# Kernel tuning notes

Hardware: AMD Instinct MI355X
Metric: run time of the kernel (lower is better)

The kernel has to match this reference:

```python
import jax, jax.numpy as jnp
import numpy as np

B, C, H, W = 8, 256, 64, 64
OUT, K = 256, 3
OG = 1
STRIDE, PAD, DIL = 1, 1, 1
K2 = K * K


def setup_inputs() -> dict:
    key = jax.random.key(0)
    ks = jax.random.split(key, 5)
    x = jax.random.normal(ks[0], (B, C, H, W), jnp.float32)
    # main deform-conv weight [out, in//groups, k, k]
    weight = jax.random.normal(ks[1], (OUT, C, K, K), jnp.float32) * (1.0 / np.sqrt(C * K2))
    bias = jax.random.normal(ks[2], (OUT,), jnp.float32) * 0.01
    # param_generator: 3x3 conv -> 3*OG*K*K channels (oh, ow, mask)
    pg_w = jax.random.normal(ks[3], (3 * OG * K2, C, 3, 3), jnp.float32) * 0.01
    pg_b = jax.random.normal(ks[4], (3 * OG * K2,), jnp.float32) * 0.01
    return {"x": x, "weight": weight, "bias": bias, "pg_w": pg_w, "pg_b": pg_b}


def _conv3x3(x, w, b):
    y = jax.lax.conv_general_dilated(
        x, w, (1, 1), [(1, 1), (1, 1)],
        dimension_numbers=("NCHW", "OIHW", "NCHW"))
    return y + b[None, :, None, None]


def _bilinear_gather(img, py, px):
    # img [B,C,H,W]; py,px [B,K2,Ho,Wo] -> [B,C,K2,Ho,Wo]
    # Zero padding outside the image (torchvision deform_conv2d semantics).
    Hh, Ww = img.shape[2], img.shape[3]
    y0 = jnp.floor(py)
    x0 = jnp.floor(px)
    dy = py - y0
    dx = px - x0
    imgf = img.reshape(img.shape[0], img.shape[1], Hh * Ww)
    out = jnp.zeros((img.shape[0], img.shape[1]) + py.shape[1:], img.dtype)
    corners = (
        (0, 0, (1 - dy) * (1 - dx)),
        (0, 1, (1 - dy) * dx),
        (1, 0, dy * (1 - dx)),
        (1, 1, dy * dx),
    )
    for oy, ox, wgt in corners:
        yy = y0 + oy
        xx = x0 + ox
        valid = (yy >= 0) & (yy < Hh) & (xx >= 0) & (xx < Ww)
        yi = jnp.clip(yy, 0, Hh - 1).astype(jnp.int32)
        xi = jnp.clip(xx, 0, Ww - 1).astype(jnp.int32)
        idx = yi * Ww + xi  # [B,K2,Ho,Wo]
        g = jax.vmap(lambda im, ix: jnp.take(im, ix.reshape(-1), axis=1))(imgf, idx)
        g = g.reshape(img.shape[0], img.shape[1], *idx.shape[1:])
        out = out + g * (wgt * valid)[:, None]
    return out


def _deform_conv2d(x, weight, bias, pg_w, pg_b):
    Bn = x.shape[0]
    Hi, Wi = x.shape[2], x.shape[3]
    Ho = (Hi + 2 * PAD - DIL * (K - 1) - 1) // STRIDE + 1
    Wo = (Wi + 2 * PAD - DIL * (K - 1) - 1) // STRIDE + 1
    params = _conv3x3(x, pg_w, pg_b)  # [B, 3*OG*K2, H, W]
    oh, ow, mask = jnp.split(params, 3, axis=1)
    offset = jnp.concatenate([oh, ow], axis=1)  # [B, 2*OG*K2, Ho, Wo]
    mask = jax.nn.sigmoid(mask)                  # [B, OG*K2, Ho, Wo]
    # torchvision layout: channel = ((og*K2 + k)*2 + {y,x})
    off = offset.reshape(Bn, OG, K2, 2, Ho, Wo)
    dy = off[:, :, :, 0].reshape(Bn, K2, Ho, Wo)  # OG == 1
    dx = off[:, :, :, 1].reshape(Bn, K2, Ho, Wo)
    hy = jnp.arange(Ho, dtype=x.dtype) * STRIDE - PAD
    wx = jnp.arange(Wo, dtype=x.dtype) * STRIDE - PAD
    ky, kx = jnp.meshgrid(jnp.arange(K), jnp.arange(K), indexing="ij")
    base_y = hy[None, :, None] + (ky.reshape(-1) * DIL).astype(x.dtype)[:, None, None]  # [K2,Ho,1]
    base_x = wx[None, None, :] + (kx.reshape(-1) * DIL).astype(x.dtype)[:, None, None]  # [K2,1,Wo]
    py = dy + base_y[None]  # [B,K2,Ho,Wo]
    px = dx + base_x[None]
    sampled = _bilinear_gather(x, py, px)          # [B,C,K2,Ho,Wo]
    sampled = sampled * mask[:, None]              # modulation (OG=1)
    out = jnp.einsum("bckhw,ock->bohw", sampled, weight.reshape(OUT, C, K2))
    return out + bias[None, :, None, None]


def reference(x, weight, bias, pg_w, pg_b):
    return _deform_conv2d(x, weight, bias, pg_w, pg_b)
```

## Files before the change

kernel.cpp:

```cpp
#include <hip/hip_runtime.h>
#include <math.h>

#define BQ   8
#define CIN  256
#define HH   64
#define WW   64
#define COUT 256
#define K2   9
#define PCH  27

#define PT     64
#define CCH    32
#define NCHUNK (CIN / CCH)
#define NSTEP  72
#define NSUB   24
#define SUBROW 104
#define PLANE  (HH * WW)

typedef __attribute__((ext_vector_type(8))) short short8;
typedef __attribute__((ext_vector_type(4))) float f32x4;
typedef __attribute__((ext_vector_type(2))) float f32x2;

#define PIPE_BARRIER() do {                                   \
    asm volatile("s_waitcnt lgkmcnt(0)" ::: "memory");        \
    __builtin_amdgcn_s_barrier();                             \
    asm volatile("" ::: "memory");                            \
} while (0)

static __device__ __forceinline__ unsigned short f2bf(float f) {
    unsigned u = __builtin_bit_cast(unsigned, f);
    u += 0x7fff + ((u >> 16) & 1);
    return (unsigned short)(u >> 16);
}
static __device__ __forceinline__ f32x2 up2(unsigned u) {
    f32x2 r;
    r[0] = __builtin_bit_cast(float, u << 16);
    r[1] = __builtin_bit_cast(float, u & 0xffff0000u);
    return r;
}
static __device__ __forceinline__ unsigned cvtpk(float lo, float hi) {
    unsigned r;
    asm("v_cvt_pk_bf16_f32 %0, %1, %2" : "=v"(r) : "v"(lo), "v"(hi));
    return r;
}

__global__ __launch_bounds__(256) void k_packw(const float* __restrict__ w,
                                               unsigned short* __restrict__ wp) {
    int t = blockIdx.x * 256 + threadIdx.x;
    if (t >= NSTEP * COUT * 4) return;
    int q = t & 3;
    int o = (t >> 2) & 255;
    int s = t >> 10;
    short8 sv;
#pragma unroll
    for (int j = 0; j < 8; ++j) {
        int pos   = s * 32 + q * 8 + j;
        int chunk = pos / (CCH * K2);
        int pl    = pos % (CCH * K2);
        int ktap  = pl >> 5;
        int c     = chunk * CCH + (pl & 31);
        sv[j] = (short)f2bf(w[(o * CIN + c) * K2 + ktap]);
    }
    *(short8*)(wp + (size_t)t * 8) = sv;
}

__global__ __launch_bounds__(256) void k_packpg(const float* __restrict__ pgw,
                                                unsigned short* __restrict__ wpg) {
    int t = blockIdx.x * 256 + threadIdx.x;
    if (t >= NSTEP * 32 * 4) return;
    int q = t & 3;
    int o = (t >> 2) & 31;
    int s = t >> 7;
    short8 sv;
#pragma unroll
    for (int j = 0; j < 8; ++j) {
        int pos   = s * 32 + q * 8 + j;
        int chunk = pos / (CCH * K2);
        int pl    = pos % (CCH * K2);
        int ktap  = pl >> 5;
        int c     = chunk * CCH + (pl & 31);
        sv[j] = (o < PCH) ? (short)f2bf(pgw[(size_t)(o * CIN + c) * K2 + ktap]) : (short)0;
    }
    *(short8*)(wpg + (size_t)t * 8) = sv;
}

__global__ __launch_bounds__(256) void k_xt(const float* __restrict__ x,
                                            unsigned short* __restrict__ xT) {
    __shared__ float tile[64][65];
    int blk = blockIdx.x;
    int cc  = blk & 3;
    int y   = (blk >> 2) & 63;
    int b   = blk >> 8;
    int t   = threadIdx.x;
    int c0  = cc * 64;

    const float* xp = x + ((size_t)(b * CIN + c0) * HH + y) * WW;
#pragma unroll
    for (int r = 0; r < 16; ++r) {
        int cl = r * 4 + (t >> 6);
        int xx = t & 63;
        tile[cl][xx] = xp[(size_t)cl * PLANE + xx];
    }
    __syncthreads();
    unsigned short* op = xT + ((size_t)b * PLANE + (size_t)y * WW) * CIN + c0;
#pragma unroll
    for (int r = 0; r < 16; ++r) {
        int xx = r * 4 + (t >> 6);
        int cl = t & 63;
        op[(size_t)xx * CIN + cl] = f2bf(tile[cl][xx]);
    }
}

__global__ __launch_bounds__(512, 4) void k_fused(const unsigned short* __restrict__ xT,
                                                  const unsigned short* __restrict__ wp,
                                                  const unsigned short* __restrict__ wpg,
                                                  const float* __restrict__ bias,
                                                  const float* __restrict__ pgb,
                                                  float* __restrict__ out) {
    __shared__ alignas(16) unsigned short s_samp[2][PT][SUBROW];
    __shared__ float4 s_wgt4[K2][PT];
    __shared__ int4   s_off4[K2][PT];
    __shared__ float  s_params[32][65];

    int blk = blockIdx.x;
    int swz = (blk & 7) * 64 + (blk >> 3);
    int b   = swz >> 6;
    int h   = swz & 63;
    int t   = threadIdx.x;

    int gp = t >> 3;
    int cg = t & 7;
    int wv = t >> 6;
    int lm = t & 15;
    int lq = (t >> 4) & 3;

    const char* xTb = (const char*)xT + (size_t)b * PLANE * CIN * 2;

    {
        int ipg = wv >> 2;
        int rpg = wv & 3;
        f32x4 accA = (f32x4){0.f, 0.f, 0.f, 0.f};
        f32x4 accB = (f32x4){0.f, 0.f, 0.f, 0.f};

        int  pixo[K2];
        bool okk[K2];
#pragma unroll
        for (int k = 0; k < K2; ++k) {
            int row = h + (k / 3) - 1;
            int col = gp + (k % 3) - 1;
            okk[k]  = ((unsigned)row < (unsigned)HH) & ((unsigned)col < (unsigned)WW);
            int pix = min(max(row, 0), HH - 1) * WW + min(max(col, 0), WW - 1);
            pixo[k] = pix * (CIN * 2) + cg * 8;
        }

        uint2 Ga[3];
#pragma unroll
        for (int j = 0; j < 3; ++j)
            Ga[j] = *(const uint2*)(xTb + pixo[j]);
#pragma unroll
        for (int j = 0; j < 3; ++j) {
            uint2 d = Ga[j];
            if (!okk[j]) { d.x = 0; d.y = 0; }
            *(uint2*)&s_samp[0][gp][j * 32 + cg * 4] = d;
        }
#pragma unroll
        for (int j = 0; j < 3; ++j)
            Ga[j] = *(const uint2*)(xTb + pixo[3 + j]);
        PIPE_BARRIER();

        short8 ac = *(const short8*)(wpg + (ipg * 16 + lm) * 32 + lq * 8);
        for (int sc = 0; sc < NSUB; ++sc) {
            bool doC = (sc + 1 < NSUB);
            bool doL = (sc + 2 < NSUB);
            int t1 = ((sc + 1) % 3) * 3;
            int t2 = ((sc + 2) % 3) * 3;
            int c2 = ((sc + 2) / 3) * (CCH * 2);
            unsigned short (*__restrict__ bc)[SUBROW] = s_samp[sc & 1];
            unsigned short (*__restrict__ bn)[SUBROW] = s_samp[(sc + 1) & 1];
#pragma unroll
            for (int sl = 0; sl < 3; ++sl) {
                short8 bf = *(const short8*)&bc[rpg * 16 + lm][sl * 32 + lq * 8];
                int r = sc * 3 + sl + 1;
                short8 an = ac;
                if (r < NSTEP)
                    an = *(const short8*)(wpg + (size_t)r * 32 * 32
                                          + (ipg * 16 + lm) * 32 + lq * 8);
                if (doC) {
                    uint2 d = Ga[sl];
                    if (!okk[t1 + sl]) { d.x = 0; d.y = 0; }
                    *(uint2*)&bn[gp][sl * 32 + cg * 4] = d;
                }
                if (doL)
                    Ga[sl] = *(const uint2*)(xTb + pixo[t2 + sl] + c2);
                if (sl & 1)
                    accB = __builtin_amdgcn_mfma_f32_16x16x32_bf16(ac, bf, accB, 0, 0, 0);
                else
                    accA = __builtin_amdgcn_mfma_f32_16x16x32_bf16(ac, bf, accA, 0, 0, 0);
                ac = an;
            }
            PIPE_BARRIER();
        }
        f32x4 accpg = accA + accB;
#pragma unroll
        for (int rg = 0; rg < 4; ++rg) {
            int oc = ipg * 16 + lq * 4 + rg;
            float bb = (oc < PCH) ? pgb[oc] : 0.f;
            s_params[oc][rpg * 16 + lm] = accpg[rg] + bb;
        }
    }
    __syncthreads();

    for (int e = t; e < K2 * PT; e += 512) {
        int k = e >> 6;
        int p = e & 63;
        float dy = s_params[2 * k][p];
        float dx = s_params[2 * k + 1][p];
        float mz = s_params[18 + k][p];
        float m  = 1.f / (1.f + expf(-mz));

        float py = dy + (float)(h - 1 + k / 3);
        float px = dx + (float)(p - 1 + k % 3);
        float y0f = floorf(py), x0f = floorf(px);
        float fy = py - y0f,    fx = px - x0f;
        int iy0 = (int)y0f, ix0 = (int)x0f;
        int iy1 = iy0 + 1,  ix1 = ix0 + 1;
        bool vy0 = (unsigned)iy0 < (unsigned)HH;
        bool vy1 = (unsigned)iy1 < (unsigned)HH;
        bool vx0 = (unsigned)ix0 < (unsigned)WW;
        bool vx1 = (unsigned)ix1 < (unsigned)WW;

        float w00 = (1.f - fy) * (1.f - fx) * m; if (!(vy0 && vx0)) w00 = 0.f;
        float w01 = (1.f - fy) * fx         * m; if (!(vy0 && vx1)) w01 = 0.f;
        float w10 = fy         * (1.f - fx) * m; if (!(vy1 && vx0)) w10 = 0.f;
        float w11 = fy         * fx         * m; if (!(vy1 && vx1)) w11 = 0.f;

        int cy0 = min(max(iy0, 0), HH - 1), cy1 = min(max(iy1, 0), HH - 1);
        int cx0 = min(max(ix0, 0), WW - 1), cx1 = min(max(ix1, 0), WW - 1);

        s_wgt4[k][p] = make_float4(w00, w01, w10, w11);
        s_off4[k][p] = make_int4((cy0 * WW + cx0) * 512, (cy0 * WW + cx1) * 512,
                                 (cy1 * WW + cx0) * 512, (cy1 * WW + cx1) * 512);
    }
    __syncthreads();

    int ow = wv * 32;
    f32x4 acc[2][4];
#pragma unroll
    for (int i = 0; i < 2; ++i)
#pragma unroll
        for (int j = 0; j < 4; ++j) acc[i][j] = (f32x4){0.f, 0.f, 0.f, 0.f};

    uint2 G[3][4];
    {
#pragma unroll
        for (int j = 0; j < 3; ++j) {
            int4 ob = s_off4[j][gp];
            G[j][0] = *(const uint2*)(xTb + ob.x + cg * 8);
            G[j][1] = *(const uint2*)(xTb + ob.y + cg * 8);
            G[j][2] = *(const uint2*)(xTb + ob.z + cg * 8);
            G[j][3] = *(const uint2*)(xTb + ob.w + cg * 8);
        }
#pragma unroll
        for (int j = 0; j < 3; ++j) {
            float4 gw = s_wgt4[j][gp];
            f32x2 v01 = gw.x * up2(G[j][0].x) + gw.y * up2(G[j][1].x)
                      + gw.z * up2(G[j][2].x) + gw.w * up2(G[j][3].x);
            f32x2 v23 = gw.x * up2(G[j][0].y) + gw.y * up2(G[j][1].y)
                      + gw.z * up2(G[j][2].y) + gw.w * up2(G[j][3].y);
            uint2 pk;
            pk.x = cvtpk(v01[0], v01[1]);
            pk.y = cvtpk(v23[0], v23[1]);
            *(uint2*)&s_samp[0][gp][j * 32 + cg * 4] = pk;
        }
#pragma unroll
        for (int j = 0; j < 3; ++j) {
            int4 ob = s_off4[3 + j][gp];
            G[j][0] = *(const uint2*)(xTb + ob.x + cg * 8);
            G[j][1] = *(const uint2*)(xTb + ob.y + cg * 8);
            G[j][2] = *(const uint2*)(xTb + ob.z + cg * 8);
            G[j][3] = *(const uint2*)(xTb + ob.w + cg * 8);
        }
        PIPE_BARRIER();
    }

    short8 a0c = *(const short8*)(wp + (ow +  0 + lm) * 32 + lq * 8);
    short8 a1c = *(const short8*)(wp + (ow + 16 + lm) * 32 + lq * 8);
    for (int sc = 0; sc < NSUB; ++sc) {
        bool doC = (sc + 1 < NSUB);
        bool doL = (sc + 2 < NSUB);
        int t1 = ((sc + 1) % 3) * 3;
        int t2 = ((sc + 2) % 3) * 3;
        int c2 = ((sc + 2) / 3) * (CCH * 2) + cg * 8;
        unsigned short (*__restrict__ bc)[SUBROW] = s_samp[sc & 1];
        unsigned short (*__restrict__ bn)[SUBROW] = s_samp[(sc + 1) & 1];
#pragma unroll
        for (int sl = 0; sl < 3; ++sl) {
            short8 b0 = *(const short8*)&bc[ 0 + lm][sl * 32 + lq * 8];
            short8 b1 = *(const short8*)&bc[16 + lm][sl * 32 + lq * 8];
            short8 b2 = *(const short8*)&bc[32 + lm][sl * 32 + lq * 8];
            short8 b3 = *(const short8*)&bc[48 + lm][sl * 32 + lq * 8];
            int r = sc * 3 + sl + 1;
            short8 a0n = a0c, a1n = a1c;
            if (r < NSTEP) {
                const unsigned short* wrn = wp + (size_t)r * COUT * 32;
                a0n = *(const short8*)(wrn + (ow +  0 + lm) * 32 + lq * 8);
                a1n = *(const short8*)(wrn + (ow + 16 + lm) * 32 + lq * 8);
            }
            if (doC) {
                float4 gw = s_wgt4[t1 + sl][gp];
                f32x2 v01 = gw.x * up2(G[sl][0].x) + gw.y * up2(G[sl][1].x)
                          + gw.z * up2(G[sl][2].x) + gw.w * up2(G[sl][3].x);
                f32x2 v23 = gw.x * up2(G[sl][0].y) + gw.y * up2(G[sl][1].y)
                          + gw.z * up2(G[sl][2].y) + gw.w * up2(G[sl][3].y);
                uint2 pk;
                pk.x = cvtpk(v01[0], v01[1]);
                pk.y = cvtpk(v23[0], v23[1]);
                *(uint2*)&bn[gp][sl * 32 + cg * 4] = pk;
            }
            if (doL) {
                int4 ob = s_off4[t2 + sl][gp];
                G[sl][0] = *(const uint2*)(xTb + ob.x + c2);
                G[sl][1] = *(const uint2*)(xTb + ob.y + c2);
                G[sl][2] = *(const uint2*)(xTb + ob.z + c2);
                G[sl][3] = *(const uint2*)(xTb + ob.w + c2);
            }
            __builtin_amdgcn_s_setprio(1);
            acc[0][0] = __builtin_amdgcn_mfma_f32_16x16x32_bf16(a0c, b0, acc[0][0], 0, 0, 0);
            acc[0][1] = __builtin_amdgcn_mfma_f32_16x16x32_bf16(a0c, b1, acc[0][1], 0, 0, 0);
            acc[0][2] = __builtin_amdgcn_mfma_f32_16x16x32_bf16(a0c, b2, acc[0][2], 0, 0, 0);
            acc[0][3] = __builtin_amdgcn_mfma_f32_16x16x32_bf16(a0c, b3, acc[0][3], 0, 0, 0);
            acc[1][0] = __builtin_amdgcn_mfma_f32_16x16x32_bf16(a1c, b0, acc[1][0], 0, 0, 0);
            acc[1][1] = __builtin_amdgcn_mfma_f32_16x16x32_bf16(a1c, b1, acc[1][1], 0, 0, 0);
            acc[1][2] = __builtin_amdgcn_mfma_f32_16x16x32_bf16(a1c, b2, acc[1][2], 0, 0, 0);
            acc[1][3] = __builtin_amdgcn_mfma_f32_16x16x32_bf16(a1c, b3, acc[1][3], 0, 0, 0);
            __builtin_amdgcn_s_setprio(0);
            a0c = a0n; a1c = a1n;
        }
        PIPE_BARRIER();
    }

    float* op = out + ((size_t)b * COUT) * PLANE + h * WW;
#pragma unroll
    for (int i = 0; i < 2; ++i) {
        int o0 = ow + i * 16 + lq * 4;
        f32x4 bv = *(const f32x4*)(bias + o0);
#pragma unroll
        for (int rg = 0; rg < 4; ++rg) {
#pragma unroll
            for (int j = 0; j < 4; ++j)
                op[(size_t)(o0 + rg) * PLANE + j * 16 + lm] = acc[i][j][rg] + bv[rg];
        }
    }
}

extern "C" void kernel_launch(void* const* d_in, const int* in_sizes, int n_in,
                              void* d_out, int out_size, void* d_ws, size_t ws_size,
                              hipStream_t stream) {
    const float* x    = (const float*)d_in[0];
    const float* wgt  = (const float*)d_in[1];
    const float* bias = (const float*)d_in[2];
    const float* pgw  = (const float*)d_in[3];
    const float* pgb  = (const float*)d_in[4];
    float* out = (float*)d_out;

    const size_t WPK_B = (size_t)NSTEP * COUT * 32 * 2;
    const size_t WPG_B = (size_t)NSTEP * 32 * 32 * 2;
    unsigned short* wpk = (unsigned short*)d_ws;
    unsigned short* wpg = (unsigned short*)((char*)d_ws + WPK_B);
    unsigned short* xT  = (unsigned short*)((char*)d_ws + WPK_B + WPG_B);

    k_packw <<<(NSTEP * COUT * 4 + 255) / 256, 256, 0, stream>>>(wgt, wpk);
    k_packpg<<<(NSTEP * 32 * 4 + 255) / 256,   256, 0, stream>>>(pgw, wpg);
    k_xt    <<<BQ * HH * 4, 256, 0, stream>>>(x, xT);
    k_fused <<<BQ * HH, 512, 0, stream>>>(xT, wpk, wpg, bias, pgb, out);
}
```

Before: 120.2 us.

## Retile MFMA warp tiles to 64 outputs x 32 pixels and shrink gather registers

Each wave now covers 64 output channels by 32 pixels instead of 32 by 64. That cuts LDS B-fragment reads per step but doubles the weight A-fragment global loads, which are no longer prefetched one step ahead. The bilinear weights are hoisted into registers, and the gather buffer is cut from three sets of corner loads to one, with a reordered loop. The aim is lower register pressure and LDS traffic. The cost is gather and weight-load latency that is less hidden behind the MFMAs.

```diff
diff --git a/kernel.cpp b/kernel.cpp
--- a/kernel.cpp
+++ b/kernel.cpp
@@ -243,111 +243,125 @@
     }
     __syncthreads();
 
-    int ow = wv * 32;
-    f32x4 acc[2][4];
-#pragma unroll
-    for (int i = 0; i < 2; ++i)
-#pragma unroll
-        for (int j = 0; j < 4; ++j) acc[i][j] = (f32x4){0.f, 0.f, 0.f, 0.f};
-
-    uint2 G[3][4];
+    int ow  = (wv >> 1) * 64;
+    int pxt = (wv & 1) * 32;
+    f32x4 acc[4][2];
+#pragma unroll
+    for (int i = 0; i < 4; ++i)
+#pragma unroll
+        for (int j = 0; j < 2; ++j) acc[i][j] = (f32x4){0.f, 0.f, 0.f, 0.f};
+
+    f32x4 wreg[K2];
+#pragma unroll
+    for (int k = 0; k < K2; ++k)
+        wreg[k] = *(const f32x4*)&s_wgt4[k][gp];
+
+    uint2 G[4];
     {
+        uint2 Gp[3][4];
 #pragma unroll
         for (int j = 0; j < 3; ++j) {
             int4 ob = s_off4[j][gp];
-            G[j][0] = *(const uint2*)(xTb + ob.x + cg * 8);
-            G[j][1] = *(const uint2*)(xTb + ob.y + cg * 8);
-            G[j][2] = *(const uint2*)(xTb + ob.z + cg * 8);
-            G[j][3] = *(const uint2*)(xTb + ob.w + cg * 8);
+            Gp[j][0] = *(const uint2*)(xTb + ob.x + cg * 8);
+            Gp[j][1] = *(const uint2*)(xTb + ob.y + cg * 8);
+            Gp[j][2] = *(const uint2*)(xTb + ob.z + cg * 8);
+            Gp[j][3] = *(const uint2*)(xTb + ob.w + cg * 8);
         }
 #pragma unroll
         for (int j = 0; j < 3; ++j) {
-            float4 gw = s_wgt4[j][gp];
-            f32x2 v01 = gw.x * up2(G[j][0].x) + gw.y * up2(G[j][1].x)
-                      + gw.z * up2(G[j][2].x) + gw.w * up2(G[j][3].x);
-            f32x2 v23 = gw.x * up2(G[j][0].y) + gw.y * up2(G[j][1].y)
-                      + gw.z * up2(G[j][2].y) + gw.w * up2(G[j][3].y);
+            f32x4 gw = wreg[j];
+            f32x2 v01 = gw[0] * up2(Gp[j][0].x) + gw[1] * up2(Gp[j][1].x)
+                      + gw[2] * up2(Gp[j][2].x) + gw[3] * up2(Gp[j][3].x);
+            f32x2 v23 = gw[0] * up2(Gp[j][0].y) + gw[1] * up2(Gp[j][1].y)
+                      + gw[2] * up2(Gp[j][2].y) + gw[3] * up2(Gp[j][3].y);
             uint2 pk;
             pk.x = cvtpk(v01[0], v01[1]);
             pk.y = cvtpk(v23[0], v23[1]);
             *(uint2*)&s_samp[0][gp][j * 32 + cg * 4] = pk;
         }
-#pragma unroll
-        for (int j = 0; j < 3; ++j) {
-            int4 ob = s_off4[3 + j][gp];
-            G[j][0] = *(const uint2*)(xTb + ob.x + cg * 8);
-            G[j][1] = *(const uint2*)(xTb + ob.y + cg * 8);
-            G[j][2] = *(const uint2*)(xTb + ob.z + cg * 8);
-            G[j][3] = *(const uint2*)(xTb + ob.w + cg * 8);
+        {
+            int4 ob = s_off4[3][gp];
+            G[0] = *(const uint2*)(xTb + ob.x + cg * 8);
+            G[1] = *(const uint2*)(xTb + ob.y + cg * 8);
+            G[2] = *(const uint2*)(xTb + ob.z + cg * 8);
+            G[3] = *(const uint2*)(xTb + ob.w + cg * 8);
         }
         PIPE_BARRIER();
     }
 
-    short8 a0c = *(const short8*)(wp + (ow +  0 + lm) * 32 + lq * 8);
-    short8 a1c = *(const short8*)(wp + (ow + 16 + lm) * 32 + lq * 8);
-    for (int sc = 0; sc < NSUB; ++sc) {
-        bool doC = (sc + 1 < NSUB);
-        bool doL = (sc + 2 < NSUB);
-        int t1 = ((sc + 1) % 3) * 3;
-        int t2 = ((sc + 2) % 3) * 3;
-        int c2 = ((sc + 2) / 3) * (CCH * 2) + cg * 8;
-        unsigned short (*__restrict__ bc)[SUBROW] = s_samp[sc & 1];
-        unsigned short (*__restrict__ bn)[SUBROW] = s_samp[(sc + 1) & 1];
-#pragma unroll
-        for (int sl = 0; sl < 3; ++sl) {
-            short8 b0 = *(const short8*)&bc[ 0 + lm][sl * 32 + lq * 8];
-            short8 b1 = *(const short8*)&bc[16 + lm][sl * 32 + lq * 8];
-            short8 b2 = *(const short8*)&bc[32 + lm][sl * 32 + lq * 8];
-            short8 b3 = *(const short8*)&bc[48 + lm][sl * 32 + lq * 8];
-            int r = sc * 3 + sl + 1;
-            short8 a0n = a0c, a1n = a1c;
-            if (r < NSTEP) {
-                const unsigned short* wrn = wp + (size_t)r * COUT * 32;
-                a0n = *(const short8*)(wrn + (ow +  0 + lm) * 32 + lq * 8);
-                a1n = *(const short8*)(wrn + (ow + 16 + lm) * 32 + lq * 8);
+    for (int ch = 0; ch < NCHUNK; ++ch) {
+        const int chb = ch * (CCH * 2);
+#pragma unroll
+        for (int q = 0; q < 3; ++q) {
+            unsigned short (*__restrict__ bc)[SUBROW] = s_samp[(ch + q) & 1];
+            unsigned short (*__restrict__ bn)[SUBROW] = s_samp[(ch + q + 1) & 1];
+            const int T1 = ((q + 1) % 3) * 3;
+            const int cC = chb + ((q + 1) / 3) * (CCH * 2);
+            const int T2 = ((q + 2) % 3) * 3;
+            const int cL = chb + ((q + 2) / 3) * (CCH * 2);
+            const bool doC = (q < 2) || (ch < NCHUNK - 1);
+            const bool doL2 = (ch * 3 + q + 2) < NSUB;
+#pragma unroll
+            for (int sl = 0; sl < 3; ++sl) {
+                short8 b0 = *(const short8*)&bc[pxt +  0 + lm][sl * 32 + lq * 8];
+                short8 b1 = *(const short8*)&bc[pxt + 16 + lm][sl * 32 + lq * 8];
+                const unsigned short* wr = wp + (size_t)(ch * 9 + q * 3 + sl) * COUT * 32;
+                short8 a0 = *(const short8*)(wr + (ow +  0 + lm) * 32 + lq * 8);
+                short8 a1 = *(const short8*)(wr + (ow + 16 + lm) * 32 + lq * 8);
+                short8 a2 = *(const short8*)(wr + (ow + 32 + lm) * 32 + lq * 8);
+                short8 a3 = *(const short8*)(wr + (ow + 48 + lm) * 32 + lq * 8);
+                if (doC) {
+                    f32x4 gw = wreg[T1 + sl];
+                    f32x2 v01 = gw[0] * up2(G[0].x) + gw[1] * up2(G[1].x)
+                              + gw[2] * up2(G[2].x) + gw[3] * up2(G[3].x);
+                    f32x2 v23 = gw[0] * up2(G[0].y) + gw[1] * up2(G[1].y)
+                              + gw[2] * up2(G[2].y) + gw[3] * up2(G[3].y);
+                    uint2 pk;
+                    pk.x = cvtpk(v01[0], v01[1]);
+                    pk.y = cvtpk(v23[0], v23[1]);
+                    *(uint2*)&bn[gp][sl * 32 + cg * 4] = pk;
+                }
+                if (sl < 2) {
+                    if (doC) {
+                        int4 ob = s_off4[T1 + sl + 1][gp];
+                        G[0] = *(const uint2*)(xTb + ob.x + cC + cg * 8);
+                        G[1] = *(const uint2*)(xTb + ob.y + cC + cg * 8);
+                        G[2] = *(const uint2*)(xTb + ob.z + cC + cg * 8);
+                        G[3] = *(const uint2*)(xTb + ob.w + cC + cg * 8);
+                    }
+                } else {
+                    if (doL2) {
+                        int4 ob = s_off4[T2][gp];
+                        G[0] = *(const uint2*)(xTb + ob.x + cL + cg * 8);
+                        G[1] = *(const uint2*)(xTb + ob.y + cL + cg * 8);
+                        G[2] = *(const uint2*)(xTb + ob.z + cL + cg * 8);
+                        G[3] = *(const uint2*)(xTb + ob.w + cL + cg * 8);
+                    }
+                }
+                __builtin_amdgcn_s_setprio(1);
+                acc[0][0] = __builtin_amdgcn_mfma_f32_16x16x32_bf16(a0, b0, acc[0][0], 0, 0, 0);
+                acc[0][1] = __builtin_amdgcn_mfma_f32_16x16x32_bf16(a0, b1, acc[0][1], 0, 0, 0);
+                acc[1][0] = __builtin_amdgcn_mfma_f32_16x16x32_bf16(a1, b0, acc[1][0], 0, 0, 0);
+                acc[1][1] = __builtin_amdgcn_mfma_f32_16x16x32_bf16(a1, b1, acc[1][1], 0, 0, 0);
+                acc[2][0] = __builtin_amdgcn_mfma_f32_16x16x32_bf16(a2, b0, acc[2][0], 0, 0, 0);
+                acc[2][1] = __builtin_amdgcn_mfma_f32_16x16x32_bf16(a2, b1, acc[2][1], 0, 0, 0);
+                acc[3][0] = __builtin_amdgcn_mfma_f32_16x16x32_bf16(a3, b0, acc[3][0], 0, 0, 0);
+                acc[3][1] = __builtin_amdgcn_mfma_f32_16x16x32_bf16(a3, b1, acc[3][1], 0, 0, 0);
+                __builtin_amdgcn_s_setprio(0);
             }
-            if (doC) {
-                float4 gw = s_wgt4[t1 + sl][gp];
-                f32x2 v01 = gw.x * up2(G[sl][0].x) + gw.y * up2(G[sl][1].x)
-                          + gw.z * up2(G[sl][2].x) + gw.w * up2(G[sl][3].x);
-                f32x2 v23 = gw.x * up2(G[sl][0].y) + gw.y * up2(G[sl][1].y)
-                          + gw.z * up2(G[sl][2].y) + gw.w * up2(G[sl][3].y);
-                uint2 pk;
-                pk.x = cvtpk(v01[0], v01[1]);
-                pk.y = cvtpk(v23[0], v23[1]);
-                *(uint2*)&bn[gp][sl * 32 + cg * 4] = pk;
-            }
-            if (doL) {
-                int4 ob = s_off4[t2 + sl][gp];
-                G[sl][0] = *(const uint2*)(xTb + ob.x + c2);
-                G[sl][1] = *(const uint2*)(xTb + ob.y + c2);
-                G[sl][2] = *(const uint2*)(xTb + ob.z + c2);
-                G[sl][3] = *(const uint2*)(xTb + ob.w + c2);
-            }
-            __builtin_amdgcn_s_setprio(1);
-            acc[0][0] = __builtin_amdgcn_mfma_f32_16x16x32_bf16(a0c, b0, acc[0][0], 0, 0, 0);
-            acc[0][1] = __builtin_amdgcn_mfma_f32_16x16x32_bf16(a0c, b1, acc[0][1], 0, 0, 0);
-            acc[0][2] = __builtin_amdgcn_mfma_f32_16x16x32_bf16(a0c, b2, acc[0][2], 0, 0, 0);
-            acc[0][3] = __builtin_amdgcn_mfma_f32_16x16x32_bf16(a0c, b3, acc[0][3], 0, 0, 0);
-            acc[1][0] = __builtin_amdgcn_mfma_f32_16x16x32_bf16(a1c, b0, acc[1][0], 0, 0, 0);
-            acc[1][1] = __builtin_amdgcn_mfma_f32_16x16x32_bf16(a1c, b1, acc[1][1], 0, 0, 0);
-            acc[1][2] = __builtin_amdgcn_mfma_f32_16x16x32_bf16(a1c, b2, acc[1][2], 0, 0, 0);
-            acc[1][3] = __builtin_amdgcn_mfma_f32_16x16x32_bf16(a1c, b3, acc[1][3], 0, 0, 0);
-            __builtin_amdgcn_s_setprio(0);
-            a0c = a0n; a1c = a1n;
-        }
-        PIPE_BARRIER();
-    }
-
-    float* op = out + ((size_t)b * COUT) * PLANE + h * WW;
-#pragma unroll
-    for (int i = 0; i < 2; ++i) {
+            PIPE_BARRIER();
+        }
+    }
+
+    float* op = out + ((size_t)b * COUT) * PLANE + h * WW + pxt;
+#pragma unroll
+    for (int i = 0; i < 4; ++i) {
         int o0 = ow + i * 16 + lq * 4;
         f32x4 bv = *(const f32x4*)(bias + o0);
 #pragma unroll
         for (int rg = 0; rg < 4; ++rg) {
 #pragma unroll
-            for (int j = 0; j < 4; ++j)
+            for (int j = 0; j < 2; ++j)
                 op[(size_t)(o0 + rg) * PLANE + j * 16 + lm] = acc[i][j][rg] + bv[rg];
         }
     }
```

Result: slower. 177.4 us (+47.6%).

## Split offset/mask param conv into separate kernel with row-tile LDS reuse

Applied to the files above, without the earlier changes.

Moves the 3x3 parameter-generator convolution out of the fused deform-conv kernel into its own kernel that writes offsets and mask logits to a global workspace. The new kernel loads three halo-padded input rows per channel chunk into LDS once and reuses them across all nine taps, instead of gathering each tap separately. The main kernel then reads the parameters from global memory. This lowers LDS and register pressure in the fused kernel and cuts redundant gathers, at the cost of an extra launch, a global round trip for the parameters, and a simpler unpipelined loop in the new kernel.

```diff
diff --git a/kernel.cpp b/kernel.cpp
--- a/kernel.cpp
+++ b/kernel.cpp
@@ -111,16 +111,11 @@
     }
 }
 
-__global__ __launch_bounds__(512, 4) void k_fused(const unsigned short* __restrict__ xT,
-                                                  const unsigned short* __restrict__ wp,
-                                                  const unsigned short* __restrict__ wpg,
-                                                  const float* __restrict__ bias,
-                                                  const float* __restrict__ pgb,
-                                                  float* __restrict__ out) {
-    __shared__ alignas(16) unsigned short s_samp[2][PT][SUBROW];
-    __shared__ float4 s_wgt4[K2][PT];
-    __shared__ int4   s_off4[K2][PT];
-    __shared__ float  s_params[32][65];
+__global__ __launch_bounds__(512, 4) void k_params(const unsigned short* __restrict__ xT,
+                                                   const unsigned short* __restrict__ wpg,
+                                                   const float* __restrict__ pgb,
+                                                   float* __restrict__ pv) {
+    __shared__ alignas(16) unsigned short s_rows[3][66][40];
 
     int blk = blockIdx.x;
     int swz = (blk & 7) * 64 + (blk >> 3);
@@ -128,6 +123,79 @@
     int h   = swz & 63;
     int t   = threadIdx.x;
 
+    int wv  = t >> 6;
+    int lm  = t & 15;
+    int lq  = (t >> 4) & 3;
+    int ipg = wv >> 2;
+    int rpg = wv & 3;
+
+    const unsigned short* xTb = xT + (size_t)b * PLANE * CIN;
+
+    if (t < 24) {
+        int ky  = t >> 3;
+        int rem = t & 7;
+        int col = (rem >> 2) * 65;
+        int q   = rem & 3;
+        uint4 z = make_uint4(0, 0, 0, 0);
+        *(uint4*)&s_rows[ky][col][q * 8] = z;
+    }
+    __syncthreads();
+
+    f32x4 accA = (f32x4){0.f, 0.f, 0.f, 0.f};
+    f32x4 accB = (f32x4){0.f, 0.f, 0.f, 0.f};
+
+    int pxm1 = t >> 3;
+    int cgs  = (t & 7) * 4;
+
+    for (int ch = 0; ch < NCHUNK; ++ch) {
+#pragma unroll
+        for (int ky = 0; ky < 3; ++ky) {
+            int y = h + ky - 1;
+            uint2 d = make_uint2(0, 0);
+            if ((unsigned)y < (unsigned)HH)
+                d = *(const uint2*)(xTb + (size_t)(y * WW + pxm1) * CIN + ch * CCH + cgs);
+            *(uint2*)&s_rows[ky][pxm1 + 1][cgs] = d;
+        }
+        __syncthreads();
+#pragma unroll
+        for (int tap = 0; tap < K2; ++tap) {
+            int ky = tap / 3, kx = tap % 3;
+            short8 a  = *(const short8*)(wpg + (size_t)(ch * K2 + tap) * 32 * 32
+                                         + (ipg * 16 + lm) * 32 + lq * 8);
+            short8 bf = *(const short8*)&s_rows[ky][rpg * 16 + lm + kx][lq * 8];
+            if (tap & 1)
+                accB = __builtin_amdgcn_mfma_f32_16x16x32_bf16(a, bf, accB, 0, 0, 0);
+            else
+                accA = __builtin_amdgcn_mfma_f32_16x16x32_bf16(a, bf, accA, 0, 0, 0);
+        }
+        __syncthreads();
+    }
+
+    f32x4 accpg = accA + accB;
+    int px = rpg * 16 + lm;
+#pragma unroll
+    for (int rg = 0; rg < 4; ++rg) {
+        int oc = ipg * 16 + lq * 4 + rg;
+        if (oc < PCH)
+            pv[((size_t)(b * PCH + oc) << 12) + h * WW + px] = accpg[rg] + pgb[oc];
+    }
+}
+
+__global__ __launch_bounds__(512, 4) void k_fused(const unsigned short* __restrict__ xT,
+                                                  const unsigned short* __restrict__ wp,
+                                                  const float* __restrict__ pv,
+                                                  const float* __restrict__ bias,
+                                                  float* __restrict__ out) {
+    __shared__ alignas(16) unsigned short s_samp[2][PT][SUBROW];
+    __shared__ float4 s_wgt4[K2][PT];
+    __shared__ int4   s_off4[K2][PT];
+
+    int blk = blockIdx.x;
+    int swz = (blk & 7) * 64 + (blk >> 3);
+    int b   = swz >> 6;
+    int h   = swz & 63;
+    int t   = threadIdx.x;
+
     int gp = t >> 3;
     int cg = t & 7;
     int wv = t >> 6;
@@ -136,86 +204,13 @@
 
     const char* xTb = (const char*)xT + (size_t)b * PLANE * CIN * 2;
 
-    {
-        int ipg = wv >> 2;
-        int rpg = wv & 3;
-        f32x4 accA = (f32x4){0.f, 0.f, 0.f, 0.f};
-        f32x4 accB = (f32x4){0.f, 0.f, 0.f, 0.f};
-
-        int  pixo[K2];
-        bool okk[K2];
-#pragma unroll
-        for (int k = 0; k < K2; ++k) {
-            int row = h + (k / 3) - 1;
-            int col = gp + (k % 3) - 1;
-            okk[k]  = ((unsigned)row < (unsigned)HH) & ((unsigned)col < (unsigned)WW);
-            int pix = min(max(row, 0), HH - 1) * WW + min(max(col, 0), WW - 1);
-            pixo[k] = pix * (CIN * 2) + cg * 8;
-        }
-
-        uint2 Ga[3];
-#pragma unroll
-        for (int j = 0; j < 3; ++j)
-            Ga[j] = *(const uint2*)(xTb + pixo[j]);
-#pragma unroll
-        for (int j = 0; j < 3; ++j) {
-            uint2 d = Ga[j];
-            if (!okk[j]) { d.x = 0; d.y = 0; }
-            *(uint2*)&s_samp[0][gp][j * 32 + cg * 4] = d;
-        }
-#pragma unroll
-        for (int j = 0; j < 3; ++j)
-            Ga[j] = *(const uint2*)(xTb + pixo[3 + j]);
-        PIPE_BARRIER();
-
-        short8 ac = *(const short8*)(wpg + (ipg * 16 + lm) * 32 + lq * 8);
-        for (int sc = 0; sc < NSUB; ++sc) {
-            bool doC = (sc + 1 < NSUB);
-            bool doL = (sc + 2 < NSUB);
-            int t1 = ((sc + 1) % 3) * 3;
-            int t2 = ((sc + 2) % 3) * 3;
-            int c2 = ((sc + 2) / 3) * (CCH * 2);
-            unsigned short (*__restrict__ bc)[SUBROW] = s_samp[sc & 1];
-            unsigned short (*__restrict__ bn)[SUBROW] = s_samp[(sc + 1) & 1];
-#pragma unroll
-            for (int sl = 0; sl < 3; ++sl) {
-                short8 bf = *(const short8*)&bc[rpg * 16 + lm][sl * 32 + lq * 8];
-                int r = sc * 3 + sl + 1;
-                short8 an = ac;
-                if (r < NSTEP)
-                    an = *(const short8*)(wpg + (size_t)r * 32 * 32
-                                          + (ipg * 16 + lm) * 32 + lq * 8);
-                if (doC) {
-                    uint2 d = Ga[sl];
-                    if (!okk[t1 + sl]) { d.x = 0; d.y = 0; }
-                    *(uint2*)&bn[gp][sl * 32 + cg * 4] = d;
-                }
-                if (doL)
-                    Ga[sl] = *(const uint2*)(xTb + pixo[t2 + sl] + c2);
-                if (sl & 1)
-                    accB = __builtin_amdgcn_mfma_f32_16x16x32_bf16(ac, bf, accB, 0, 0, 0);
-                else
-                    accA = __builtin_amdgcn_mfma_f32_16x16x32_bf16(ac, bf, accA, 0, 0, 0);
-                ac = an;
-            }
-            PIPE_BARRIER();
-        }
-        f32x4 accpg = accA + accB;
-#pragma unroll
-        for (int rg = 0; rg < 4; ++rg) {
-            int oc = ipg * 16 + lq * 4 + rg;
-            float bb = (oc < PCH) ? pgb[oc] : 0.f;
-            s_params[oc][rpg * 16 + lm] = accpg[rg] + bb;
-        }
-    }
-    __syncthreads();
-
+    const float* pvb = pv + ((size_t)(b * PCH) << 12) + h * WW;
     for (int e = t; e < K2 * PT; e += 512) {
         int k = e >> 6;
         int p = e & 63;
-        float dy = s_params[2 * k][p];
-        float dx = s_params[2 * k + 1][p];
-        float mz = s_params[18 + k][p];
+        float dy = pvb[(size_t)(2 * k) << 12 | (unsigned)p];
+        float dx = pvb[(size_t)(2 * k + 1) << 12 | (unsigned)p];
+        float mz = pvb[(size_t)(18 + k) << 12 | (unsigned)p];
         float m  = 1.f / (1.f + expf(-mz));
 
         float py = dy + (float)(h - 1 + k / 3);
@@ -365,12 +360,15 @@
 
     const size_t WPK_B = (size_t)NSTEP * COUT * 32 * 2;
     const size_t WPG_B = (size_t)NSTEP * 32 * 32 * 2;
+    const size_t XT_B  = (size_t)BQ * PLANE * CIN * 2;
     unsigned short* wpk = (unsigned short*)d_ws;
     unsigned short* wpg = (unsigned short*)((char*)d_ws + WPK_B);
     unsigned short* xT  = (unsigned short*)((char*)d_ws + WPK_B + WPG_B);
+    float*          pv  = (float*)((char*)d_ws + WPK_B + WPG_B + XT_B);
 
     k_packw <<<(NSTEP * COUT * 4 + 255) / 256, 256, 0, stream>>>(wgt, wpk);
     k_packpg<<<(NSTEP * 32 * 4 + 255) / 256,   256, 0, stream>>>(pgw, wpg);
     k_xt    <<<BQ * HH * 4, 256, 0, stream>>>(x, xT);
-    k_fused <<<BQ * HH, 512, 0, stream>>>(xT, wpk, wpg, bias, pgb, out);
-}
+    k_params<<<BQ * HH, 512, 0, stream>>>(xT, wpg, pgb, pv);
+    k_fused <<<BQ * HH, 512, 0, stream>>>(xT, wpk, pv, bias, out);
+}
```

Result: no change. 118.7 us (-1.2%).
